# Performance work log

Measured on AMD Instinct MI355X. Metric: run time of the kernel, lower is better.

Reference implementation:

```python
import jax, jax.numpy as jnp
import numpy as np

D = 4  # search range -> 2*D+1 = 9 correlation channels


def setup_inputs() -> dict:
    key = jax.random.key(0)
    k1, k2 = jax.random.split(key)
    N, C, H, W = 4, 128, 192, 640
    feature1 = jax.random.normal(k1, (N, C, H, W), dtype=jnp.float32)
    feature2 = jax.random.normal(k2, (N, C, H, W), dtype=jnp.float32)
    return {"feature1": feature1, "feature2": feature2}


def reference(feature1, feature2):
    # feature1, feature2: [N, C, H, W]
    N, C, H, W = feature1.shape
    d = D
    # Pad feature2 along width: [N, C, H, W + 2d]
    f2p = jnp.pad(feature2, ((0, 0), (0, 0), (0, 0), (d, d)))
    # For each shift i in [0, 2d], correlate feature1 with f2p[..., i:i+W]
    # and take the channel mean -> [N, 1, H, W]; concatenate over shifts.
    costs = [
        jnp.mean(feature1 * jax.lax.dynamic_slice_in_dim(f2p, i, W, axis=3),
                 axis=1, keepdims=True)
        for i in range(2 * d + 1)
    ]
    return jnp.concatenate(costs, axis=1)  # [N, 2d+1, H, W]
```

## Files before the change

### kernel.cpp

```cpp
#include <hip/hip_runtime.h>


constexpr int DD = 4;
constexpr int NSHIFT = 2 * DD + 1;
constexpr int N_ = 4, C_ = 128, H_ = 192, W_ = 640;

__global__ __launch_bounds__(320)
void cost_volume_kernel(const float* __restrict__ f1,
                        const float* __restrict__ f2,
                        float* __restrict__ out)
{
    constexpr int HW = H_ * W_;
    const int t   = threadIdx.x;
    const int row = blockIdx.x;
    const int n   = row / H_;
    const int h   = row - n * H_;

    const float* f1row = f1 + (size_t)n * C_ * HW + (size_t)h * W_;
    const float* f2row = f2 + (size_t)n * C_ * HW + (size_t)h * W_;

    __shared__ float s[2][W_ + 2 * DD];

    if (t < DD) {
        s[0][t] = 0.f;            s[1][t] = 0.f;
        s[0][DD + W_ + t] = 0.f;  s[1][DD + W_ + t] = 0.f;
    }

    const int w = 2 * t;
    float acc0[NSHIFT], acc1[NSHIFT];
#pragma unroll
    for (int i = 0; i < NSHIFT; ++i) { acc0[i] = 0.f; acc1[i] = 0.f; }

    float2 a = *(const float2*)(f1row + w);
    {
        float2 b0 = *(const float2*)(f2row + w);
        *(float2*)&s[0][DD + w] = b0;
    }
    __syncthreads();

    int p = 0;
    for (int c = 0; c < C_ - 1; ++c) {
        const float2 b_n = *(const float2*)(f2row + (size_t)(c + 1) * HW + w);
        const float2 a_n = *(const float2*)(f1row + (size_t)(c + 1) * HW + w);

        float v[NSHIFT + 1];
        const float* sp = &s[p][w];
#pragma unroll
        for (int i = 0; i < 5; ++i)
            *(float2*)&v[2 * i] = *(const float2*)(sp + 2 * i);
#pragma unroll
        for (int i = 0; i < NSHIFT; ++i) {
            acc0[i] = fmaf(a.x, v[i],     acc0[i]);
            acc1[i] = fmaf(a.y, v[i + 1], acc1[i]);
        }

        *(float2*)&s[p ^ 1][DD + w] = b_n;
        __syncthreads();
        a = a_n;
        p ^= 1;
    }

    {
        float v[NSHIFT + 1];
        const float* sp = &s[p][w];
#pragma unroll
        for (int i = 0; i < 5; ++i)
            *(float2*)&v[2 * i] = *(const float2*)(sp + 2 * i);
#pragma unroll
        for (int i = 0; i < NSHIFT; ++i) {
            acc0[i] = fmaf(a.x, v[i],     acc0[i]);
            acc1[i] = fmaf(a.y, v[i + 1], acc1[i]);
        }
    }

    constexpr float scale = 1.0f / (float)C_;
    float* orow = out + (size_t)n * NSHIFT * HW + (size_t)h * W_ + w;
#pragma unroll
    for (int i = 0; i < NSHIFT; ++i) {
        float2 o;
        o.x = acc0[i] * scale;
        o.y = acc1[i] * scale;
        *(float2*)(orow + (size_t)i * HW) = o;
    }
}

extern "C" void kernel_launch(void* const* d_in, const int* in_sizes, int n_in,
                              void* d_out, int out_size, void* d_ws, size_t ws_size,
                              hipStream_t stream) {
    const float* f1 = (const float*)d_in[0];
    const float* f2 = (const float*)d_in[1];
    float* out = (float*)d_out;
    dim3 grid(N_ * H_);
    dim3 block(320);
    cost_volume_kernel<<<grid, block, 0, stream>>>(f1, f2, out);
}
```

Before: 479.9 us.

## Replace shared-memory row staging with per-wave register prefetch of shifted loads

Each 64-lane wave now owns a 128-column segment of one row. It loads the shifted feature2 windows directly from global memory into registers, with a two-stage register prefetch, so the shared-memory buffer and the per-channel __syncthreads are gone. The cost is redundant global loads, five float2 windows per lane per channel instead of one, which rely on L1/L2 to absorb the overlap. Padding is handled with bounds predicates, and the grid changes to 256-thread blocks of four independent waves.

```diff
diff --git a/kernel.cpp b/kernel.cpp
--- a/kernel.cpp
+++ b/kernel.cpp
@@ -2,81 +2,76 @@
 
 
 constexpr int DD = 4;
-constexpr int NSHIFT = 2 * DD + 1;
+constexpr int NS = 2 * DD + 1;
 constexpr int N_ = 4, C_ = 128, H_ = 192, W_ = 640;
+constexpr int HW = H_ * W_;
+constexpr int SEGS  = W_ / 128;
+constexpr int TILES = N_ * H_ * SEGS;
+constexpr int WPB   = 4;
+constexpr int NBLK  = TILES / WPB;
 
-__global__ __launch_bounds__(320)
+__global__ __launch_bounds__(256)
 void cost_volume_kernel(const float* __restrict__ f1,
                         const float* __restrict__ f2,
                         float* __restrict__ out)
 {
-    constexpr int HW = H_ * W_;
-    const int t   = threadIdx.x;
-    const int row = blockIdx.x;
-    const int n   = row / H_;
-    const int h   = row - n * H_;
+    const int lane = threadIdx.x & 63;
+    const int wid  = blockIdx.x * WPB + (threadIdx.x >> 6);
+    const int seg  = wid % SEGS;
+    const int row  = wid / SEGS;
+    const int n    = row / H_;
+    const int h    = row - n * H_;
+    const int w0   = seg * 128 + lane * 2;
 
-    const float* f1row = f1 + (size_t)n * C_ * HW + (size_t)h * W_;
-    const float* f2row = f2 + (size_t)n * C_ * HW + (size_t)h * W_;
+    const size_t base = (size_t)n * C_ * HW + (size_t)h * W_;
+    const float* f1p = f1 + base + w0;
+    const float* f2p = f2 + base;
 
-    __shared__ float s[2][W_ + 2 * DD];
+    float2 A[2];
+    float2 B[2][5];
 
-    if (t < DD) {
-        s[0][t] = 0.f;            s[1][t] = 0.f;
-        s[0][DD + W_ + t] = 0.f;  s[1][DD + W_ + t] = 0.f;
-    }
+    auto load_stage = [&](int st, int c) {
+        const float* f1c = f1p + (size_t)c * HW;
+        const float* f2c = f2p + (size_t)c * HW;
+        A[st] = *(const float2*)f1c;
+#pragma unroll
+        for (int k = 0; k < 5; ++k) {
+            const int off = w0 - 4 + 2 * k;
+            float2 v = make_float2(0.f, 0.f);
+            if ((unsigned)off <= (unsigned)(W_ - 2))
+                v = *(const float2*)(f2c + off);
+            B[st][k] = v;
+        }
+    };
 
-    const int w = 2 * t;
-    float acc0[NSHIFT], acc1[NSHIFT];
+    float acc0[NS], acc1[NS];
 #pragma unroll
-    for (int i = 0; i < NSHIFT; ++i) { acc0[i] = 0.f; acc1[i] = 0.f; }
+    for (int i = 0; i < NS; ++i) { acc0[i] = 0.f; acc1[i] = 0.f; }
 
-    float2 a = *(const float2*)(f1row + w);
-    {
-        float2 b0 = *(const float2*)(f2row + w);
-        *(float2*)&s[0][DD + w] = b0;
-    }
-    __syncthreads();
+    load_stage(0, 0);
+    load_stage(1, 1);
 
-    int p = 0;
-    for (int c = 0; c < C_ - 1; ++c) {
-        const float2 b_n = *(const float2*)(f2row + (size_t)(c + 1) * HW + w);
-        const float2 a_n = *(const float2*)(f1row + (size_t)(c + 1) * HW + w);
+#pragma unroll 2
+    for (int c = 0; c < C_; ++c) {
+        const int st = c & 1;
+        const float2 a = A[st];
+        float v[10];
+#pragma unroll
+        for (int k = 0; k < 5; ++k) { v[2*k] = B[st][k].x; v[2*k+1] = B[st][k].y; }
 
-        float v[NSHIFT + 1];
-        const float* sp = &s[p][w];
 #pragma unroll
-        for (int i = 0; i < 5; ++i)
-            *(float2*)&v[2 * i] = *(const float2*)(sp + 2 * i);
-#pragma unroll
-        for (int i = 0; i < NSHIFT; ++i) {
+        for (int i = 0; i < NS; ++i) {
             acc0[i] = fmaf(a.x, v[i],     acc0[i]);
             acc1[i] = fmaf(a.y, v[i + 1], acc1[i]);
         }
 
-        *(float2*)&s[p ^ 1][DD + w] = b_n;
-        __syncthreads();
-        a = a_n;
-        p ^= 1;
-    }
-
-    {
-        float v[NSHIFT + 1];
-        const float* sp = &s[p][w];
-#pragma unroll
-        for (int i = 0; i < 5; ++i)
-            *(float2*)&v[2 * i] = *(const float2*)(sp + 2 * i);
-#pragma unroll
-        for (int i = 0; i < NSHIFT; ++i) {
-            acc0[i] = fmaf(a.x, v[i],     acc0[i]);
-            acc1[i] = fmaf(a.y, v[i + 1], acc1[i]);
-        }
+        if (c + 2 < C_) load_stage(st, c + 2);
     }
 
     constexpr float scale = 1.0f / (float)C_;
-    float* orow = out + (size_t)n * NSHIFT * HW + (size_t)h * W_ + w;
+    float* orow = out + (size_t)n * NS * HW + (size_t)h * W_ + w0;
 #pragma unroll
-    for (int i = 0; i < NSHIFT; ++i) {
+    for (int i = 0; i < NS; ++i) {
         float2 o;
         o.x = acc0[i] * scale;
         o.y = acc1[i] * scale;
@@ -90,7 +85,5 @@
     const float* f1 = (const float*)d_in[0];
     const float* f2 = (const float*)d_in[1];
     float* out = (float*)d_out;
-    dim3 grid(N_ * H_);
-    dim3 block(320);
-    cost_volume_kernel<<<grid, block, 0, stream>>>(f1, f2, out);
+    cost_volume_kernel<<<dim3(NBLK), dim3(256), 0, stream>>>(f1, f2, out);
 }
```

Result: slower. 518.0 us (+7.9%).
